# Optimization experiments

Hardware: AMD Instinct MI355X
Metric: run time of the kernel (lower is better)

Reference implementation:

```python
import jax, jax.numpy as jnp
import numpy as np

IMG_H, IMG_W = 800, 1344
STRIDE = 16
FH, FW = IMG_H // STRIDE, IMG_W // STRIDE  # 50, 84
C = 1024
N_PROP = 3000
K_KEEP = 512          # post-NMS proposals kept by merge_proposals
POOL = 14             # C4 ROI-align output resolution
NMS_THRESH = 0.7
NUM_CLASSES = 80


def _make_boxes(key, n):
    r = jax.random.uniform(key, (n, 4))
    cx = r[:, 0] * IMG_W
    cy = r[:, 1] * IMG_H
    w = 16.0 + r[:, 2] * 480.0
    h = 16.0 + r[:, 3] * 480.0
    x0 = jnp.clip(cx - w / 2, 0.0, IMG_W)
    y0 = jnp.clip(cy - h / 2, 0.0, IMG_H)
    x1 = jnp.clip(cx + w / 2, 0.0, IMG_W)
    y1 = jnp.clip(cy + h / 2, 0.0, IMG_H)
    return jnp.stack([x0, y0, x1, y1], axis=-1)


def setup_inputs() -> dict:
    key = jax.random.key(0)
    ks = jax.random.split(key, 14)
    feat = jax.random.normal(ks[0], (C, FH, FW), jnp.float32)
    boxes1 = _make_boxes(ks[1], N_PROP)
    boxes2 = _make_boxes(ks[2], N_PROP)
    logits1 = jax.random.normal(ks[3], (N_PROP,), jnp.float32)
    logits2 = jax.random.normal(ks[4], (N_PROP,), jnp.float32)
    levels1 = jnp.zeros((N_PROP,), jnp.int32)  # single C4 level
    levels2 = jnp.zeros((N_PROP,), jnp.int32)
    scale1 = 1.0 + 0.02 * jax.random.normal(ks[5], (C,), jnp.float32)
    bias1 = 0.02 * jax.random.normal(ks[6], (C,), jnp.float32)
    scale2 = 1.0 + 0.02 * jax.random.normal(ks[7], (C,), jnp.float32)
    bias2 = 0.02 * jax.random.normal(ks[8], (C,), jnp.float32)
    W_cls1 = 0.01 * jax.random.normal(ks[9], (C, NUM_CLASSES + 1), jnp.float32)
    b_cls1 = jnp.zeros((NUM_CLASSES + 1,), jnp.float32)
    W_box1 = 0.001 * jax.random.normal(ks[10], (C, NUM_CLASSES * 4), jnp.float32)
    b_box1 = jnp.zeros((NUM_CLASSES * 4,), jnp.float32)
    W_cls2 = 0.01 * jax.random.normal(ks[11], (C, NUM_CLASSES + 1), jnp.float32)
    b_cls2 = jnp.zeros((NUM_CLASSES + 1,), jnp.float32)
    W_box2 = 0.001 * jax.random.normal(ks[12], (C, NUM_CLASSES * 4), jnp.float32)
    b_box2 = jnp.zeros((NUM_CLASSES * 4,), jnp.float32)
    return dict(feat=feat, boxes1=boxes1, boxes2=boxes2, logits1=logits1,
                logits2=logits2, levels1=levels1, levels2=levels2,
                scale1=scale1, bias1=bias1, scale2=scale2, bias2=bias2,
                W_cls1=W_cls1, b_cls1=b_cls1, W_box1=W_box1, b_box1=b_box1,
                W_cls2=W_cls2, b_cls2=b_cls2, W_box2=W_box2, b_box2=b_box2)


def _clip_boxes(boxes):
    return jnp.stack([jnp.clip(boxes[:, 0], 0.0, IMG_W),
                      jnp.clip(boxes[:, 1], 0.0, IMG_H),
                      jnp.clip(boxes[:, 2], 0.0, IMG_W),
                      jnp.clip(boxes[:, 3], 0.0, IMG_H)], axis=-1)


def _nms(boxes, scores, k, thresh):
    """Greedy NMS; returns k kept indices (fixed-size, jit-friendly)."""
    areas = (boxes[:, 2] - boxes[:, 0]) * (boxes[:, 3] - boxes[:, 1])

    def body(i, state):
        sw, keep = state
        idx = jnp.argmax(sw)
        keep = keep.at[i].set(idx.astype(jnp.int32))
        b = boxes[idx]
        ix0 = jnp.maximum(b[0], boxes[:, 0])
        iy0 = jnp.maximum(b[1], boxes[:, 1])
        ix1 = jnp.minimum(b[2], boxes[:, 2])
        iy1 = jnp.minimum(b[3], boxes[:, 3])
        inter = jnp.maximum(ix1 - ix0, 0.0) * jnp.maximum(iy1 - iy0, 0.0)
        iou = inter / (areas[idx] + areas - inter + 1e-9)
        sw = jnp.where(iou > thresh, -jnp.inf, sw)
        sw = sw.at[idx].set(-jnp.inf)
        return sw, keep

    keep0 = jnp.zeros((k,), jnp.int32)
    _, keep = jax.lax.fori_loop(0, k, body, (scores, keep0))
    return keep


def _roi_align(feat, boxes, spatial_scale, pool):
    """ROIAlign (aligned=True, sampling_ratio=1). feat [C,H,W], boxes [R,4] -> [R,C,pool,pool]."""
    Cc, H, W = feat.shape
    b = boxes * spatial_scale - 0.5
    x0, y0, x1, y1 = b[:, 0], b[:, 1], b[:, 2], b[:, 3]
    bw = (x1 - x0) / pool
    bh = (y1 - y0) / pool
    grid = jnp.arange(pool, dtype=feat.dtype) + 0.5
    xs = x0[:, None] + grid[None, :] * bw[:, None]  # [R,P]
    ys = y0[:, None] + grid[None, :] * bh[:, None]  # [R,P]
    yf = jnp.floor(ys); xf = jnp.floor(xs)
    ly = ys - yf; lx = xs - xf
    y0c = jnp.clip(yf.astype(jnp.int32), 0, H - 1)
    y1c = jnp.clip(yf.astype(jnp.int32) + 1, 0, H - 1)
    x0c = jnp.clip(xf.astype(jnp.int32), 0, W - 1)
    x1c = jnp.clip(xf.astype(jnp.int32) + 1, 0, W - 1)

    def g(Y, X):  # gather -> [C,R,P,P]
        return feat[:, Y[:, :, None], X[:, None, :]]

    wy0 = (1.0 - ly); wy1 = ly  # [R,P]
    wx0 = (1.0 - lx); wx1 = lx
    out = (g(y0c, x0c) * (wy0[:, :, None] * wx0[:, None, :])
           + g(y0c, x1c) * (wy0[:, :, None] * wx1[:, None, :])
           + g(y1c, x0c) * (wy1[:, :, None] * wx0[:, None, :])
           + g(y1c, x1c) * (wy1[:, :, None] * wx1[:, None, :]))
    return jnp.transpose(out, (1, 0, 2, 3))  # [R,C,P,P]


def _box_head(roi_feats, scale, bias, W_cls, b_cls, W_box, b_box):
    bf = roi_feats * scale[None, :, None, None] + bias[None, :, None, None]
    x = bf.mean(axis=(2, 3))  # [R,C]
    return bf, x @ W_cls + b_cls, x @ W_box + b_box


def reference(feat, boxes1, boxes2, logits1, logits2, levels1, levels2,
              scale1, bias1, scale2, bias2,
              W_cls1, b_cls1, W_box1, b_box1,
              W_cls2, b_cls2, W_box2, b_box2):
    boxes = _clip_boxes(jnp.concatenate([boxes1, boxes2], axis=0))
    scores = jnp.concatenate([logits1, logits2], axis=0)
    levels = jnp.concatenate([levels1, levels2], axis=0)
    # batched_nms level-offset trick (all zeros for single C4 level)
    off = levels.astype(boxes.dtype)[:, None] * float(max(IMG_H, IMG_W) + 1)
    keep = _nms(boxes + off, scores, K_KEEP, NMS_THRESH)
    prop = boxes[keep]  # [K,4] merged proposals

    roi = _roi_align(feat, prop, 1.0 / STRIDE, POOL)  # [K,C,P,P]
    bf1, s1, d1 = _box_head(roi, scale1, bias1, W_cls1, b_cls1, W_box1, b_box1)
    bf2, s2, d2 = _box_head(roi, scale2, bias2, W_cls2, b_cls2, W_box2, b_box2)
    return (bf1, bf2, s1, s2, d1, prop, feat)
```

## Files before the change

### kernel.cpp

```cpp
#include <hip/hip_runtime.h>

#define FHH 50
#define FWW 84
#define HW 4200
#define NBOX 6000
#define NPAD 6144
#define KKEEP 512
#define WSTRIDE 192

typedef float f32x2 __attribute__((ext_vector_type(2)));
typedef _Float16 f16x4 __attribute__((ext_vector_type(4)));
typedef _Float16 f16x2 __attribute__((ext_vector_type(2)));

#define OFF_BF1  0ULL
#define OFF_BF2  102760448ULL
#define OFF_S1   205520896ULL
#define OFF_S2   205562368ULL
#define OFF_D1   205603840ULL
#define OFF_PROP 205767680ULL
#define OFF_FEAT 205769728ULL

__global__ __launch_bounds__(256) void k_transpose(const float* __restrict__ feat,
                                                   _Float16* __restrict__ featH,
                                                   float* __restrict__ out_feat) {
  __shared__ float t[32][33];
  int hw0 = blockIdx.x * 32;
  int c0  = blockIdx.y * 32;
  int tx = threadIdx.x & 31, ty = threadIdx.x >> 5;
#pragma unroll
  for (int p = 0; p < 4; ++p) {
    int c = c0 + ty + p * 8;
    int hw = hw0 + tx;
    if (hw < HW) {
      float v = feat[(size_t)c * HW + hw];
      t[ty + p * 8][tx] = v;
      __builtin_nontemporal_store(v, &out_feat[(size_t)c * HW + hw]);
    }
  }
  __syncthreads();
#pragma unroll
  for (int p = 0; p < 4; ++p) {
    int hw = hw0 + ty + p * 8;
    int c = c0 + tx;
    if (hw < HW) featH[((size_t)hw << 10) + c] = (_Float16)t[tx][ty + p * 8];
  }
}

__global__ __launch_bounds__(256) void k_prep(const float4* __restrict__ boxes1,
                                              const float4* __restrict__ boxes2,
                                              const float* __restrict__ logits1,
                                              const float* __restrict__ logits2,
                                              const int* __restrict__ levels1,
                                              const int* __restrict__ levels2,
                                              float4* __restrict__ nbox,
                                              float* __restrict__ area,
                                              unsigned long long* __restrict__ keys,
                                              int* __restrict__ rank) {
  int i = blockIdx.x * 256 + threadIdx.x;
  if (i >= NPAD) return;
  if (i >= NBOX) { keys[i] = 0ULL; return; }
  rank[i] = 0;
  float4 b; float sc; int lv;
  if (i < 3000) { b = boxes1[i]; sc = logits1[i]; lv = levels1[i]; }
  else          { b = boxes2[i - 3000]; sc = logits2[i - 3000]; lv = levels2[i - 3000]; }
  float x0 = fminf(fmaxf(b.x, 0.f), 1344.f);
  float y0 = fminf(fmaxf(b.y, 0.f), 800.f);
  float x1 = fminf(fmaxf(b.z, 0.f), 1344.f);
  float y1 = fminf(fmaxf(b.w, 0.f), 800.f);
  float off = __fmul_rn((float)lv, 1345.0f);
  x0 = __fadd_rn(x0, off); y0 = __fadd_rn(y0, off);
  x1 = __fadd_rn(x1, off); y1 = __fadd_rn(y1, off);
  nbox[i] = make_float4(x0, y0, x1, y1);
  area[i] = __fmul_rn(__fsub_rn(x1, x0), __fsub_rn(y1, y0));
  unsigned u = __float_as_uint(sc);
  u = (u & 0x80000000u) ? ~u : (u | 0x80000000u);
  keys[i] = ((unsigned long long)u << 32) | (unsigned)(0xFFFFFFFFu - (unsigned)i);
}

__global__ __launch_bounds__(256) void k_rank(const unsigned long long* __restrict__ keys,
                                              int* __restrict__ rank) {
  __shared__ unsigned long long ks[1024];
  int jb = blockIdx.y;
  for (int t = threadIdx.x; t < 1024; t += 256) ks[t] = keys[jb * 1024 + t];
  __syncthreads();
  int i = blockIdx.x * 256 + threadIdx.x;
  if (i >= NBOX) return;
  unsigned long long ki = keys[i];
  int c = 0;
  for (int j = 0; j < 1024; ++j) c += (ks[j] > ki) ? 1 : 0;
  if (c) atomicAdd(&rank[i], c);
}

__global__ __launch_bounds__(256) void k_scatter(const float4* __restrict__ nbox,
                                                 const float* __restrict__ area,
                                                 const int* __restrict__ rank,
                                                 float4* __restrict__ sboxes,
                                                 float* __restrict__ sarea,
                                                 int* __restrict__ sorig) {
  int i = blockIdx.x * 256 + threadIdx.x;
  if (i >= NBOX) return;
  int r = rank[i];
  sboxes[r] = nbox[i];
  sarea[r] = area[i];
  sorig[r] = i;
}

__global__ __launch_bounds__(192) void k_mask(const float4* __restrict__ sboxes,
                                              const float* __restrict__ sarea,
                                              unsigned* __restrict__ mask) {
  int i0 = blockIdx.x * 4;
  int w = threadIdx.x;
  float4 b0 = sboxes[i0 + 0], b1 = sboxes[i0 + 1], b2 = sboxes[i0 + 2], b3 = sboxes[i0 + 3];
  float a0 = sarea[i0 + 0], a1 = sarea[i0 + 1], a2 = sarea[i0 + 2], a3 = sarea[i0 + 3];
  unsigned m0 = 0, m1 = 0, m2 = 0, m3 = 0;
  int jbase = w * 32;
  for (int bb = 0; bb < 32; ++bb) {
    int j = jbase + bb;
    if (j >= NBOX) break;
    float4 bj = sboxes[j];
    float aj = sarea[j];
#define IOU_BIT(BR, AR, MR)                                                          \
    {                                                                                \
      float ix0 = fmaxf(BR.x, bj.x), iy0 = fmaxf(BR.y, bj.y);                        \
      float ix1 = fminf(BR.z, bj.z), iy1 = fminf(BR.w, bj.w);                        \
      float iw = fmaxf(__fsub_rn(ix1, ix0), 0.f), ih = fmaxf(__fsub_rn(iy1, iy0), 0.f); \
      float inter = __fmul_rn(iw, ih);                                               \
      float den = __fadd_rn(__fsub_rn(__fadd_rn(AR, aj), inter), 1e-9f);             \
      float iou = __fdiv_rn(inter, den);                                             \
      if (iou > 0.7f) MR |= (1u << bb);                                              \
    }
    IOU_BIT(b0, a0, m0) IOU_BIT(b1, a1, m1) IOU_BIT(b2, a2, m2) IOU_BIT(b3, a3, m3)
#undef IOU_BIT
  }
  mask[(size_t)(i0 + 0) * WSTRIDE + w] = m0;
  mask[(size_t)(i0 + 1) * WSTRIDE + w] = m1;
  mask[(size_t)(i0 + 2) * WSTRIDE + w] = m2;
  mask[(size_t)(i0 + 3) * WSTRIDE + w] = m3;
}

#define SCAN_CH 64
__global__ __launch_bounds__(256) void k_scan(const unsigned* __restrict__ mask,
                                              const int* __restrict__ sorig,
                                              int* __restrict__ keep) {
  __shared__ unsigned srows[2][SCAN_CH * WSTRIDE];
  __shared__ int s_sorig[2][SCAN_CH];
  __shared__ int s_done, s_kept;
  int tid = threadIdx.x;
  if (tid == 0) { s_done = 0; s_kept = 0; }
  for (int idx = tid; idx < SCAN_CH * WSTRIDE; idx += 256) srows[0][idx] = mask[idx];
  if (tid < SCAN_CH) s_sorig[0][tid] = sorig[tid];
  __syncthreads();
  unsigned r0 = 0, r1 = 0, r2 = 0;
  int lane = tid;
  int kept = 0;
  for (int g = 0; g < 94; ++g) {
    int cur = g & 1, nxt = cur ^ 1;
    if (tid >= 64) {
      int gn = g + 1;
      if (gn < 94) {
        size_t gbase = (size_t)gn * SCAN_CH * WSTRIDE;
        for (int idx = tid - 64; idx < SCAN_CH * WSTRIDE; idx += 192) {
          size_t gi = gbase + idx;
          srows[nxt][idx] = (gi < (size_t)NBOX * WSTRIDE) ? mask[gi] : 0u;
        }
        if (tid - 64 < SCAN_CH) {
          int i2 = gn * SCAN_CH + (tid - 64);
          s_sorig[nxt][tid - 64] = (i2 < NBOX) ? sorig[i2] : 0;
        }
      }
    } else {
      int base = g * SCAN_CH;
      int nrows = min(SCAN_CH, NBOX - base);
      const unsigned* sb = srows[cur];
      unsigned p0 = sb[lane], p1 = sb[64 + lane], p2 = sb[128 + lane];
      for (int rr = 0; rr < nrows; ++rr) {
        unsigned c0v = p0, c1v = p1, c2v = p2;
        int rn = (rr + 1 < nrows) ? rr + 1 : rr;
        p0 = sb[rn * WSTRIDE + lane];
        p1 = sb[rn * WSTRIDE + 64 + lane];
        p2 = sb[rn * WSTRIDE + 128 + lane];
        int i = base + rr;
        int w = i >> 5, b = i & 31;
        int wl = w & 63, wc = w >> 6;
        unsigned rsel = (wc == 0) ? r0 : ((wc == 1) ? r1 : r2);
        unsigned rw = __shfl(rsel, wl);
        if (!((rw >> b) & 1u)) {
          r0 |= c0v; r1 |= c1v; r2 |= c2v;
          if (lane == 0) keep[kept] = s_sorig[cur][rr];
          kept++;
          if (kept >= KKEEP) break;
        }
      }
      if (lane == 0) { s_kept = kept; if (kept >= KKEEP) s_done = 1; }
    }
    __syncthreads();
    if (s_done) break;
  }
  __syncthreads();
  int fk = s_kept;
  for (int k = fk + tid; k < KKEEP; k += 256) keep[k] = 0;
}

__global__ __launch_bounds__(256) void k_bilin(const int* __restrict__ keep,
                                               const float4* __restrict__ boxes1,
                                               const float4* __restrict__ boxes2,
                                               float4* __restrict__ prop,
                                               float4* __restrict__ bilinW,
                                               int4* __restrict__ bilinA) {
  int r = blockIdx.x;
  __shared__ float4 spb;
  if (threadIdx.x == 0) {
    int o = keep[r];
    float4 b = (o < 3000) ? boxes1[o] : boxes2[o - 3000];
    float4 p = make_float4(fminf(fmaxf(b.x, 0.f), 1344.f),
                           fminf(fmaxf(b.y, 0.f), 800.f),
                           fminf(fmaxf(b.z, 0.f), 1344.f),
                           fminf(fmaxf(b.w, 0.f), 800.f));
    prop[r] = p;
    spb = p;
  }
  __syncthreads();
  int bin = threadIdx.x;
  if (bin >= 196) return;
  float4 pb = spb;
  const float ss = 0.0625f;
  float x0s = pb.x * ss - 0.5f, y0s = pb.y * ss - 0.5f;
  float bw = (pb.z * ss - 0.5f - x0s) / 14.0f;
  float bh = (pb.w * ss - 0.5f - y0s) / 14.0f;
  int py = bin / 14, px = bin - py * 14;
  float xs = x0s + ((float)px + 0.5f) * bw;
  float ys = y0s + ((float)py + 0.5f) * bh;
  float xf = floorf(xs), yf = floorf(ys);
  float lx = xs - xf, ly = ys - yf;
  int ix = (int)xf, iy = (int)yf;
  int x0c = min(max(ix, 0), FWW - 1), x1c = min(max(ix + 1, 0), FWW - 1);
  int y0c = min(max(iy, 0), FHH - 1), y1c = min(max(iy + 1, 0), FHH - 1);
  float wy0 = 1.f - ly, wx0 = 1.f - lx;
  bilinW[r * 196 + bin] = make_float4(wy0 * wx0, wy0 * lx, ly * wx0, ly * lx);
  bilinA[r * 196 + bin] = make_int4((y0c * FWW + x0c) << 10, (y0c * FWW + x1c) << 10,
                                    (y1c * FWW + x0c) << 10, (y1c * FWW + x1c) << 10);
}

__global__ __launch_bounds__(256) void k_roi(const _Float16* __restrict__ featH,
                                             const float4* __restrict__ bilinW,
                                             const int4* __restrict__ bilinA,
                                             const float* __restrict__ scale1,
                                             const float* __restrict__ bias1,
                                             const float* __restrict__ scale2,
                                             const float* __restrict__ bias2,
                                             float* __restrict__ bf1,
                                             float* __restrict__ bf2,
                                             float* __restrict__ x1w,
                                             float* __restrict__ x2w) {
  __shared__ _Float16 tile[32 * 198];
  __shared__ float part2f[4 * 32];
  __shared__ float sc1[32], bi1[32], sc2[32], bi2[32];
  int bid = blockIdx.x;
  int r = bid & 511;
  int c0 = (bid >> 9) * 32;
  int tid = threadIdx.x;
  int l8 = tid & 7, bg = tid >> 3;
  if (tid < 32) {
    sc1[tid] = scale1[c0 + tid]; bi1[tid] = bias1[c0 + tid];
    sc2[tid] = scale2[c0 + tid]; bi2[tid] = bias2[c0 + tid];
  }
  const _Float16* fTb = featH + c0 + l8 * 4;
  const float4* bW = bilinW + r * 196;
  const int4* bA = bilinA + r * 196;
  float4 acc = make_float4(0.f, 0.f, 0.f, 0.f);

#define ROI_BODY(BB)                                                              \
  {                                                                               \
    float4 w = bW[BB]; int4 a = bA[BB];                                           \
    f16x4 g00 = *(const f16x4*)(fTb + a.x);                                       \
    f16x4 g01 = *(const f16x4*)(fTb + a.y);                                       \
    f16x4 g10 = *(const f16x4*)(fTb + a.z);                                       \
    f16x4 g11 = *(const f16x4*)(fTb + a.w);                                       \
    float vx = (float)g00.x * w.x + (float)g01.x * w.y + (float)g10.x * w.z + (float)g11.x * w.w; \
    float vy = (float)g00.y * w.x + (float)g01.y * w.y + (float)g10.y * w.z + (float)g11.y * w.w; \
    float vz = (float)g00.z * w.x + (float)g01.z * w.y + (float)g10.z * w.z + (float)g11.z * w.w; \
    float vw = (float)g00.w * w.x + (float)g01.w * w.y + (float)g10.w * w.z + (float)g11.w * w.w; \
    acc.x += vx; acc.y += vy; acc.z += vz; acc.w += vw;                           \
    int tb = l8 * 792 + (BB);                                                     \
    tile[tb] = (_Float16)vx; tile[tb + 198] = (_Float16)vy;                       \
    tile[tb + 396] = (_Float16)vz; tile[tb + 594] = (_Float16)vw;                 \
  }

  int bb = bg;
#pragma unroll
  for (int i = 0; i < 6; ++i, bb += 32) ROI_BODY(bb)
  if (bg < 4) ROI_BODY(192 + bg)
#undef ROI_BODY

  acc.x += __shfl_xor(acc.x, 8);  acc.y += __shfl_xor(acc.y, 8);
  acc.z += __shfl_xor(acc.z, 8);  acc.w += __shfl_xor(acc.w, 8);
  acc.x += __shfl_xor(acc.x, 16); acc.y += __shfl_xor(acc.y, 16);
  acc.z += __shfl_xor(acc.z, 16); acc.w += __shfl_xor(acc.w, 16);
  acc.x += __shfl_xor(acc.x, 32); acc.y += __shfl_xor(acc.y, 32);
  acc.z += __shfl_xor(acc.z, 32); acc.w += __shfl_xor(acc.w, 32);
  if ((tid & 63) < 8) {
    int wv = tid >> 6;
    part2f[wv * 32 + l8 * 4 + 0] = acc.x;
    part2f[wv * 32 + l8 * 4 + 1] = acc.y;
    part2f[wv * 32 + l8 * 4 + 2] = acc.z;
    part2f[wv * 32 + l8 * 4 + 3] = acc.w;
  }
  __syncthreads();
  if (tid < 32) {
    float m = ((part2f[tid] + part2f[32 + tid]) + part2f[64 + tid]) + part2f[96 + tid];
    m = m / 196.0f;
    x1w[((size_t)r << 10) + c0 + tid] = m * sc1[tid] + bi1[tid];
    x2w[((size_t)r << 10) + c0 + tid] = m * sc2[tid] + bi2[tid];
  }
  size_t ob = ((size_t)((r << 10) + c0)) * 196;
  float* b1p = bf1 + ob;
  float* b2p = bf2 + ob;
  for (int it = 0; it < 13; ++it) {
    int f2 = tid + it * 256;
    if (f2 < 3136) {
      int cl = (int)((unsigned)f2 / 98u);
      int pr = f2 - cl * 98;
      f16x2 h = *(const f16x2*)&tile[cl * 198 + 2 * pr];
      float v0 = (float)h.x, v1 = (float)h.y;
      float s1v = sc1[cl], b1v = bi1[cl], s2v = sc2[cl], b2v = bi2[cl];
      f32x2 o1 = { v0 * s1v + b1v, v1 * s1v + b1v };
      f32x2 o2 = { v0 * s2v + b2v, v1 * s2v + b2v };
      __builtin_nontemporal_store(o1, (f32x2*)(b1p + 2 * f2));
      __builtin_nontemporal_store(o2, (f32x2*)(b2p + 2 * f2));
    }
  }
}

__global__ __launch_bounds__(256) void k_gemm(const float* __restrict__ x1,
                                              const float* __restrict__ x2,
                                              const float* __restrict__ Wc1, const float* __restrict__ bc1,
                                              const float* __restrict__ Wb1, const float* __restrict__ bb1,
                                              const float* __restrict__ Wc2, const float* __restrict__ bc2,
                                              float* __restrict__ s1, float* __restrict__ d1,
                                              float* __restrict__ s2) {
  int z = blockIdx.z;
  const float* A; const float* W; const float* bias; float* out; int N;
  if (z == 0)      { A = x1; W = Wc1; bias = bc1; out = s1; N = 81; }
  else if (z == 1) { A = x1; W = Wb1; bias = bb1; out = d1; N = 320; }
  else             { A = x2; W = Wc2; bias = bc2; out = s2; N = 81; }
  int n0 = blockIdx.y * 32;
  if (n0 >= N) return;
  int m0 = blockIdx.x * 32;
  __shared__ float As[32][34];
  __shared__ float Bs[32][34];
  int tid = threadIdx.x;
  int tx = tid & 15, ty = tid >> 4;
  float acc00 = 0, acc01 = 0, acc10 = 0, acc11 = 0;
  for (int k0 = 0; k0 < 1024; k0 += 32) {
    int mm = tid >> 3, g = tid & 7;
    float4 av = *(const float4*)(A + (size_t)(m0 + mm) * 1024 + k0 + g * 4);
    As[g * 4 + 0][mm] = av.x; As[g * 4 + 1][mm] = av.y;
    As[g * 4 + 2][mm] = av.z; As[g * 4 + 3][mm] = av.w;
    int nn = tid & 31, kh = tid >> 5;
#pragma unroll
    for (int qq = 0; qq < 4; ++qq) {
      int kk = kh + 8 * qq;
      int n = n0 + nn;
      Bs[kk][nn] = (n < N) ? W[(size_t)(k0 + kk) * N + n] : 0.f;
    }
    __syncthreads();
#pragma unroll
    for (int kk = 0; kk < 32; ++kk) {
      float2 a = *(const float2*)&As[kk][2 * ty];
      float2 b = *(const float2*)&Bs[kk][2 * tx];
      acc00 += a.x * b.x; acc01 += a.x * b.y;
      acc10 += a.y * b.x; acc11 += a.y * b.y;
    }
    __syncthreads();
  }
  int m = m0 + 2 * ty, n = n0 + 2 * tx;
  if (n < N) {
    out[(size_t)m * N + n] = acc00 + bias[n];
    out[(size_t)(m + 1) * N + n] = acc10 + bias[n];
  }
  if (n + 1 < N) {
    out[(size_t)m * N + n + 1] = acc01 + bias[n + 1];
    out[(size_t)(m + 1) * N + n + 1] = acc11 + bias[n + 1];
  }
}

extern "C" void kernel_launch(void* const* d_in, const int* in_sizes, int n_in,
                              void* d_out, int out_size, void* d_ws, size_t ws_size,
                              hipStream_t stream) {
  (void)in_sizes; (void)n_in; (void)out_size; (void)ws_size;
  const float* feat    = (const float*)d_in[0];
  const float4* boxes1 = (const float4*)d_in[1];
  const float4* boxes2 = (const float4*)d_in[2];
  const float* logits1 = (const float*)d_in[3];
  const float* logits2 = (const float*)d_in[4];
  const int* levels1   = (const int*)d_in[5];
  const int* levels2   = (const int*)d_in[6];
  const float* scale1  = (const float*)d_in[7];
  const float* bias1   = (const float*)d_in[8];
  const float* scale2  = (const float*)d_in[9];
  const float* bias2   = (const float*)d_in[10];
  const float* W_cls1  = (const float*)d_in[11];
  const float* b_cls1  = (const float*)d_in[12];
  const float* W_box1  = (const float*)d_in[13];
  const float* b_box1  = (const float*)d_in[14];
  const float* W_cls2  = (const float*)d_in[15];
  const float* b_cls2  = (const float*)d_in[16];

  float* out = (float*)d_out;
  char* w = (char*)d_ws;
  _Float16* featH           = (_Float16*)(w + 0);
  unsigned long long* keys  = (unsigned long long*)(w + 17203200);
  float4* nbox              = (float4*)(w + 17252352);
  float* area               = (float*)(w + 17348352);
  int* rank                 = (int*)(w + 17372352);
  float4* sboxes            = (float4*)(w + 17396352);
  float* sarea              = (float*)(w + 17492352);
  int* sorig                = (int*)(w + 17516352);
  unsigned* mask            = (unsigned*)(w + 17540352);
  int* keep                 = (int*)(w + 22148352);
  float* x1w                = (float*)(w + 22150400);
  float* x2w                = (float*)(w + 24247552);
  float4* bilinW            = (float4*)(w + 17540352);
  int4* bilinA              = (int4*)(w + 19145984);

  k_transpose<<<dim3(132, 32), 256, 0, stream>>>(feat, featH, out + OFF_FEAT);
  k_prep<<<24, 256, 0, stream>>>(boxes1, boxes2, logits1, logits2, levels1, levels2,
                                 nbox, area, keys, rank);
  k_rank<<<dim3(24, 6), 256, 0, stream>>>(keys, rank);
  k_scatter<<<24, 256, 0, stream>>>(nbox, area, rank, sboxes, sarea, sorig);
  k_mask<<<1500, 192, 0, stream>>>(sboxes, sarea, mask);
  k_scan<<<1, 256, 0, stream>>>(mask, sorig, keep);
  k_bilin<<<512, 256, 0, stream>>>(keep, boxes1, boxes2,
                                   (float4*)(out + OFF_PROP), bilinW, bilinA);
  k_roi<<<16384, 256, 0, stream>>>(featH, bilinW, bilinA,
                                   scale1, bias1, scale2, bias2,
                                   out + OFF_BF1, out + OFF_BF2, x1w, x2w);
  k_gemm<<<dim3(16, 10, 3), 256, 0, stream>>>(x1w, x2w, W_cls1, b_cls1, W_box1, b_box1,
                                              W_cls2, b_cls2,
                                              out + OFF_S1, out + OFF_D1, out + OFF_S2);
}
```

Measured before the change: 475.5 us.

## Split ROI-align into fp16 staging kernel and streaming affine-output kernel

ROI-align is split in two. The first kernel gathers bilinear samples and writes an fp16 intermediate in output layout to the workspace. A second kernel streams that buffer and writes both scaled/biased fp32 outputs with wide nontemporal stores. The aim is fully coalesced, large-granularity writes for the two ~100MB outputs, at the cost of an extra ~200MB round trip through the workspace and one more launch. The path only runs if the workspace is large enough, otherwise the fused kernel is used.

```diff
diff --git a/kernel.cpp b/kernel.cpp
--- a/kernel.cpp
+++ b/kernel.cpp
@@ -9,6 +9,7 @@
 #define WSTRIDE 192
 
 typedef float f32x2 __attribute__((ext_vector_type(2)));
+typedef float f32x4v __attribute__((ext_vector_type(4)));
 typedef _Float16 f16x4 __attribute__((ext_vector_type(4)));
 typedef _Float16 f16x2 __attribute__((ext_vector_type(2)));
 
@@ -241,6 +242,113 @@
                                     (y1c * FWW + x0c) << 10, (y1c * FWW + x1c) << 10);
 }
 
+__global__ __launch_bounds__(256) void k_roiA(const _Float16* __restrict__ featH,
+                                              const float4* __restrict__ bilinW,
+                                              const int4* __restrict__ bilinA,
+                                              const float* __restrict__ scale1,
+                                              const float* __restrict__ bias1,
+                                              const float* __restrict__ scale2,
+                                              const float* __restrict__ bias2,
+                                              _Float16* __restrict__ roiT,
+                                              float* __restrict__ x1w,
+                                              float* __restrict__ x2w) {
+  __shared__ _Float16 tile[32 * 200];
+  __shared__ float part2f[4 * 32];
+  __shared__ float sc1[32], bi1[32], sc2[32], bi2[32];
+  int bid = blockIdx.x;
+  int r = bid & 511;
+  int c0 = (bid >> 9) * 32;
+  int tid = threadIdx.x;
+  int l8 = tid & 7, bg = tid >> 3;
+  if (tid < 32) {
+    sc1[tid] = scale1[c0 + tid]; bi1[tid] = bias1[c0 + tid];
+    sc2[tid] = scale2[c0 + tid]; bi2[tid] = bias2[c0 + tid];
+  }
+  const _Float16* fTb = featH + c0 + l8 * 4;
+  const float4* bW = bilinW + r * 196;
+  const int4* bA = bilinA + r * 196;
+  float4 acc = make_float4(0.f, 0.f, 0.f, 0.f);
+
+#define ROI_BODY(BB)                                                              \
+  {                                                                               \
+    float4 w = bW[BB]; int4 a = bA[BB];                                           \
+    f16x4 g00 = *(const f16x4*)(fTb + a.x);                                       \
+    f16x4 g01 = *(const f16x4*)(fTb + a.y);                                       \
+    f16x4 g10 = *(const f16x4*)(fTb + a.z);                                       \
+    f16x4 g11 = *(const f16x4*)(fTb + a.w);                                       \
+    float vx = (float)g00.x * w.x + (float)g01.x * w.y + (float)g10.x * w.z + (float)g11.x * w.w; \
+    float vy = (float)g00.y * w.x + (float)g01.y * w.y + (float)g10.y * w.z + (float)g11.y * w.w; \
+    float vz = (float)g00.z * w.x + (float)g01.z * w.y + (float)g10.z * w.z + (float)g11.z * w.w; \
+    float vw = (float)g00.w * w.x + (float)g01.w * w.y + (float)g10.w * w.z + (float)g11.w * w.w; \
+    acc.x += vx; acc.y += vy; acc.z += vz; acc.w += vw;                           \
+    int tb = l8 * 800 + (BB);                                                     \
+    tile[tb] = (_Float16)vx; tile[tb + 200] = (_Float16)vy;                       \
+    tile[tb + 400] = (_Float16)vz; tile[tb + 600] = (_Float16)vw;                 \
+  }
+
+  int bb = bg;
+#pragma unroll
+  for (int i = 0; i < 6; ++i, bb += 32) ROI_BODY(bb)
+  if (bg < 4) ROI_BODY(192 + bg)
+#undef ROI_BODY
+
+  acc.x += __shfl_xor(acc.x, 8);  acc.y += __shfl_xor(acc.y, 8);
+  acc.z += __shfl_xor(acc.z, 8);  acc.w += __shfl_xor(acc.w, 8);
+  acc.x += __shfl_xor(acc.x, 16); acc.y += __shfl_xor(acc.y, 16);
+  acc.z += __shfl_xor(acc.z, 16); acc.w += __shfl_xor(acc.w, 16);
+  acc.x += __shfl_xor(acc.x, 32); acc.y += __shfl_xor(acc.y, 32);
+  acc.z += __shfl_xor(acc.z, 32); acc.w += __shfl_xor(acc.w, 32);
+  if ((tid & 63) < 8) {
+    int wv = tid >> 6;
+    part2f[wv * 32 + l8 * 4 + 0] = acc.x;
+    part2f[wv * 32 + l8 * 4 + 1] = acc.y;
+    part2f[wv * 32 + l8 * 4 + 2] = acc.z;
+    part2f[wv * 32 + l8 * 4 + 3] = acc.w;
+  }
+  __syncthreads();
+  if (tid < 32) {
+    float m = ((part2f[tid] + part2f[32 + tid]) + part2f[64 + tid]) + part2f[96 + tid];
+    m = m / 196.0f;
+    x1w[((size_t)r << 10) + c0 + tid] = m * sc1[tid] + bi1[tid];
+    x2w[((size_t)r << 10) + c0 + tid] = m * sc2[tid] + bi2[tid];
+  }
+  size_t ob = ((size_t)((r << 10) + c0)) * 196;
+  _Float16* tp = roiT + ob;
+  for (int it = 0; it < 7; ++it) {
+    int q = tid + it * 256;
+    if (q < 1568) {
+      int cl = q / 49;
+      int pos = (q - cl * 49) * 4;
+      f16x4 h = *(const f16x4*)&tile[cl * 200 + pos];
+      *(f16x4*)(tp + 4 * q) = h;
+    }
+  }
+}
+
+__global__ __launch_bounds__(256) void k_roiB(const _Float16* __restrict__ roiT,
+                                              const float* __restrict__ scale1,
+                                              const float* __restrict__ bias1,
+                                              const float* __restrict__ scale2,
+                                              const float* __restrict__ bias2,
+                                              float* __restrict__ bf1,
+                                              float* __restrict__ bf2) {
+  size_t base = (size_t)blockIdx.x * 12544;
+  int cbase = blockIdx.x * 256;
+  int tid = threadIdx.x;
+  for (int it = 0; it < 49; ++it) {
+    int qib = tid + it * 256;
+    size_t Q = base + qib;
+    f16x4 h = *(const f16x4*)(roiT + 4 * Q);
+    int c = (cbase + qib / 49) & 1023;
+    float s1v = scale1[c], b1v = bias1[c], s2v = scale2[c], b2v = bias2[c];
+    float v0 = (float)h.x, v1 = (float)h.y, v2 = (float)h.z, v3 = (float)h.w;
+    f32x4v o1 = { v0 * s1v + b1v, v1 * s1v + b1v, v2 * s1v + b1v, v3 * s1v + b1v };
+    f32x4v o2 = { v0 * s2v + b2v, v1 * s2v + b2v, v2 * s2v + b2v, v3 * s2v + b2v };
+    __builtin_nontemporal_store(o1, (f32x4v*)(bf1 + 4 * Q));
+    __builtin_nontemporal_store(o2, (f32x4v*)(bf2 + 4 * Q));
+  }
+}
+
 __global__ __launch_bounds__(256) void k_roi(const _Float16* __restrict__ featH,
                                              const float4* __restrict__ bilinW,
                                              const int4* __restrict__ bilinA,
@@ -268,7 +376,6 @@
   const float4* bW = bilinW + r * 196;
   const int4* bA = bilinA + r * 196;
   float4 acc = make_float4(0.f, 0.f, 0.f, 0.f);
-
 #define ROI_BODY(BB)                                                              \
   {                                                                               \
     float4 w = bW[BB]; int4 a = bA[BB];                                           \
@@ -285,13 +392,11 @@
     tile[tb] = (_Float16)vx; tile[tb + 198] = (_Float16)vy;                       \
     tile[tb + 396] = (_Float16)vz; tile[tb + 594] = (_Float16)vw;                 \
   }
-
   int bb = bg;
 #pragma unroll
   for (int i = 0; i < 6; ++i, bb += 32) ROI_BODY(bb)
   if (bg < 4) ROI_BODY(192 + bg)
 #undef ROI_BODY
-
   acc.x += __shfl_xor(acc.x, 8);  acc.y += __shfl_xor(acc.y, 8);
   acc.z += __shfl_xor(acc.z, 8);  acc.w += __shfl_xor(acc.w, 8);
   acc.x += __shfl_xor(acc.x, 16); acc.y += __shfl_xor(acc.y, 16);
@@ -387,7 +492,7 @@
 extern "C" void kernel_launch(void* const* d_in, const int* in_sizes, int n_in,
                               void* d_out, int out_size, void* d_ws, size_t ws_size,
                               hipStream_t stream) {
-  (void)in_sizes; (void)n_in; (void)out_size; (void)ws_size;
+  (void)in_sizes; (void)n_in; (void)out_size;
   const float* feat    = (const float*)d_in[0];
   const float4* boxes1 = (const float4*)d_in[1];
   const float4* boxes2 = (const float4*)d_in[2];
@@ -422,6 +527,8 @@
   float* x2w                = (float*)(w + 24247552);
   float4* bilinW            = (float4*)(w + 17540352);
   int4* bilinA              = (int4*)(w + 19145984);
+  _Float16* roiT            = (_Float16*)(w + 26344704);
+  const size_t WS_NEEDED = 26344704ULL + 205520896ULL;
 
   k_transpose<<<dim3(132, 32), 256, 0, stream>>>(feat, featH, out + OFF_FEAT);
   k_prep<<<24, 256, 0, stream>>>(boxes1, boxes2, logits1, logits2, levels1, levels2,
@@ -432,9 +539,17 @@
   k_scan<<<1, 256, 0, stream>>>(mask, sorig, keep);
   k_bilin<<<512, 256, 0, stream>>>(keep, boxes1, boxes2,
                                    (float4*)(out + OFF_PROP), bilinW, bilinA);
-  k_roi<<<16384, 256, 0, stream>>>(featH, bilinW, bilinA,
-                                   scale1, bias1, scale2, bias2,
-                                   out + OFF_BF1, out + OFF_BF2, x1w, x2w);
+  if (ws_size >= WS_NEEDED) {
+    k_roiA<<<16384, 256, 0, stream>>>(featH, bilinW, bilinA,
+                                      scale1, bias1, scale2, bias2,
+                                      roiT, x1w, x2w);
+    k_roiB<<<2048, 256, 0, stream>>>(roiT, scale1, bias1, scale2, bias2,
+                                     out + OFF_BF1, out + OFF_BF2);
+  } else {
+    k_roi<<<16384, 256, 0, stream>>>(featH, bilinW, bilinA,
+                                     scale1, bias1, scale2, bias2,
+                                     out + OFF_BF1, out + OFF_BF2, x1w, x2w);
+  }
   k_gemm<<<dim3(16, 10, 3), 256, 0, stream>>>(x1w, x2w, W_cls1, b_cls1, W_box1, b_box1,
                                               W_cls2, b_cls2,
                                               out + OFF_S1, out + OFF_D1, out + OFF_S2);
```

After: 559.8 us. 17.7% more time.
